# Optimization experiments

Hardware: AMD Instinct MI355X
Metric: run time of the kernel (lower is better)

Reference implementation:

```python
import jax, jax.numpy as jnp
import numpy as np

B, S, D, H = 2, 2048, 1024, 16
DK = D // H  # 64


def setup_inputs() -> dict:
    key = jax.random.key(0)
    ks = jax.random.split(key, 8)
    sc = 1.0 / np.sqrt(D)
    return {
        "q": jax.random.normal(ks[0], (B, S, D), jnp.float32),
        "k": jax.random.normal(ks[1], (B, S, D), jnp.float32),
        "v": jax.random.normal(ks[2], (B, S, D), jnp.float32),
        "Wq": jax.random.normal(ks[3], (D, D), jnp.float32) * sc,
        "bq": jnp.zeros((D,), jnp.float32),
        "Wk": jax.random.normal(ks[4], (D, D), jnp.float32) * sc,
        "bk": jnp.zeros((D,), jnp.float32),
        "Wv": jax.random.normal(ks[5], (D, D), jnp.float32) * sc,
        "bv": jnp.zeros((D,), jnp.float32),
        "Wo": jax.random.normal(ks[6], (D, D), jnp.float32) * sc,
        "bo": jnp.zeros((D,), jnp.float32),
    }


def _heads(x, W, b):
    # torch nn.Linear: x @ W.T + b, then view(bs,-1,H,DK).transpose(1,2)
    bsz, seq, _ = x.shape
    y = x @ W.T + b
    return y.reshape(bsz, seq, H, DK).transpose(0, 2, 1, 3)  # [B,H,S,DK]


def reference(q, k, v, Wq, bq, Wk, bk, Wv, bv, Wo, bo):
    qh = _heads(q, Wq, bq)
    kh = _heads(k, Wk, bk)
    vh = _heads(v, Wv, bv)
    # scores: [B,H,S,S]; intended scale 1/sqrt(d_k) (source passes tensor k as d_k by mistake)
    scores = jnp.einsum("bhqd,bhkd->bhqk", qh, kh) / jnp.sqrt(jnp.float32(DK))
    attn = jax.nn.softmax(scores, axis=-1)  # dropout is identity in eval
    ctx = jnp.einsum("bhqk,bhkd->bhqd", attn, vh)  # [B,H,S,DK]
    concat = ctx.transpose(0, 2, 1, 3).reshape(-1, H * DK)  # [B*S, D] (source flattens batch+seq)
    return concat @ Wo.T + bo
```

## Files before the change

### kernel.cpp

```cpp
#include <hip/hip_runtime.h>

typedef __attribute__((ext_vector_type(4))) float f32x4;
typedef __attribute__((ext_vector_type(8))) short short8;
typedef __attribute__((ext_vector_type(4))) unsigned short u16x4;
typedef __attribute__((ext_vector_type(2))) unsigned u32x2;
typedef __attribute__((ext_vector_type(4))) unsigned u32x4;

#define DEV static __device__ __forceinline__

#define BSZ 2
#define SEQ 2048
#define DMODEL 1024
#define NH 16
#define DKH 64
#define MROWS (BSZ*SEQ)
#define HEAD_ELEMS (BSZ*NH*SEQ*DKH)
#define WMAT_ELEMS (DMODEL*DMODEL)
#define QSCALE 0.18033688011111374f

DEV unsigned short f2bf(float f) {
    unsigned u = __builtin_bit_cast(unsigned, f);
    u += 0x7FFFu + ((u >> 16) & 1u);
    return (unsigned short)(u >> 16);
}

DEV unsigned cvtpk(float a, float b) {
    unsigned r;
    asm("v_cvt_pk_bf16_f32 %0, %1, %2" : "=v"(r) : "v"(a), "v"(b));
    return r;
}

DEV float fexp2(float x) {
#if __has_builtin(__builtin_amdgcn_exp2f)
    return __builtin_amdgcn_exp2f(x);
#else
    float r;
    asm("v_exp_f32 %0, %1\n\ts_nop 0" : "=v"(r) : "v"(x));
    return r;
#endif
}

DEV void gload16(const void* g, void* l) {
    __builtin_amdgcn_global_load_lds(
        (const __attribute__((address_space(1))) void*)g,
        (__attribute__((address_space(3))) void*)l, 16, 0, 0);
}

DEV void cfence() { asm volatile("" ::: "memory"); }

__global__ __launch_bounds__(256) void convall_kernel(
    const float* __restrict__ q, const float* __restrict__ k,
    const float* __restrict__ v,
    const float* __restrict__ Wq, const float* __restrict__ Wk,
    const float* __restrict__ Wv, const float* __restrict__ Wo,
    unsigned short* __restrict__ abf, unsigned short* __restrict__ wbf)
{
    const int z = blockIdx.y;
    const int i = (blockIdx.x * 256 + threadIdx.x) * 8;
    const float* src;
    unsigned short* dst;
    if (z < 3) {
        src = ((z == 0) ? q : (z == 1) ? k : v) + i;
        dst = abf + (size_t)z * HEAD_ELEMS + i;
    } else {
        const int mi = i >> 20;
        const int off = i & (WMAT_ELEMS - 1);
        src = ((mi == 0) ? Wq : (mi == 1) ? Wk : (mi == 2) ? Wv : Wo) + off;
        dst = wbf + i;
    }
    f32x4 a = *(const f32x4*)(src);
    f32x4 b = *(const f32x4*)(src + 4);
    u32x4 o;
    o[0] = cvtpk(a[0], a[1]); o[1] = cvtpk(a[2], a[3]);
    o[2] = cvtpk(b[0], b[1]); o[3] = cvtpk(b[2], b[3]);
    *(u32x4*)(dst) = o;
}

__global__ __launch_bounds__(256) void wconv_kernel(
    const float* __restrict__ Wq, const float* __restrict__ Wk,
    const float* __restrict__ Wv, const float* __restrict__ Wo,
    unsigned short* __restrict__ dst)
{
    const int z = blockIdx.y;
    const float* src = (z == 0) ? Wq : (z == 1) ? Wk : (z == 2) ? Wv : Wo;
    const int i = (blockIdx.x * 256 + threadIdx.x) * 4;
    f32x4 v = *(const f32x4*)(src + i);
    u16x4 o;
    o[0] = f2bf(v[0]); o[1] = f2bf(v[1]); o[2] = f2bf(v[2]); o[3] = f2bf(v[3]);
    *(u16x4*)(dst + (size_t)z * WMAT_ELEMS + i) = o;
}

__global__ __launch_bounds__(256) void aconv_kernel(
    const float* __restrict__ src, unsigned short* __restrict__ dst)
{
    const int i = (blockIdx.x * 256 + threadIdx.x) * 8;
    f32x4 a = *(const f32x4*)(src + i);
    f32x4 b = *(const f32x4*)(src + i + 4);
    u32x4 o;
    o[0] = cvtpk(a[0], a[1]); o[1] = cvtpk(a[2], a[3]);
    o[2] = cvtpk(b[0], b[1]); o[3] = cvtpk(b[2], b[3]);
    *(u32x4*)(dst + i) = o;
}

__global__ __launch_bounds__(256, 3) void proj_gemm_kernel(
    const unsigned short* __restrict__ Aq, const unsigned short* __restrict__ Ak,
    const unsigned short* __restrict__ Av,
    const unsigned short* __restrict__ Wbf,
    const float* __restrict__ bq, const float* __restrict__ bk, const float* __restrict__ bvv,
    unsigned short* __restrict__ heads, int zbase)
{
    const int z = zbase + blockIdx.z;
    const unsigned short* A = (z == 0) ? Aq : (z == 1) ? Ak : Av;
    const float* bias = (z == 0) ? bq : (z == 1) ? bk : bvv;
    const unsigned short* W = Wbf + (size_t)z * WMAT_ELEMS;
    unsigned short* outp = heads + (size_t)z * HEAD_ELEMS;

    __shared__ __align__(16) unsigned short As[128 * 64];
    __shared__ __align__(16) unsigned short Bs[128 * 64];

    const int tid = threadIdx.x;
    const int lane = tid & 63;
    const int w = tid >> 6;
    const int wr = w >> 1, wc = w & 1;
    const int l15 = lane & 15, l4 = lane >> 4;
    const int m0 = blockIdx.x * 128, n0 = blockIdx.y * 128;

    f32x4 acc[4][4];
    #pragma unroll
    for (int i = 0; i < 4; i++)
        #pragma unroll
        for (int j = 0; j < 4; j++) acc[i][j] = (f32x4){0.f, 0.f, 0.f, 0.f};

    const int srow = w * 8 + (lane >> 3);
    const int ssrc = ((lane & 7) ^ (srow & 7)) * 8;
    const unsigned short* ga = A + (size_t)(m0 + srow) * DMODEL + ssrc;
    const unsigned short* gb = W + (size_t)(n0 + srow) * DMODEL + ssrc;

    for (int k0 = 0; k0 < DMODEL; k0 += 64) {
        __syncthreads();
        #pragma unroll
        for (int c = 0; c < 4; c++) {
            gload16(ga + (size_t)c * 32 * DMODEL + k0, As + (c * 4 + w) * 512);
            gload16(gb + (size_t)c * 32 * DMODEL + k0, Bs + (c * 4 + w) * 512);
        }
        __syncthreads();

        short8 af[2][4], bf[2][4];
        #pragma unroll
        for (int mi = 0; mi < 4; mi++) {
            const int r = wr * 64 + mi * 16 + l15;
            const int x = r & 7;
            const char* base = (const char*)As + r * 128;
            af[0][mi] = *(const short8*)(base + ((l4 ^ x) << 4));
            af[1][mi] = *(const short8*)(base + (((4 + l4) ^ x) << 4));
        }
        #pragma unroll
        for (int ni = 0; ni < 4; ni++) {
            const int r = wc * 64 + ni * 16 + l15;
            const int x = r & 7;
            const char* base = (const char*)Bs + r * 128;
            bf[0][ni] = *(const short8*)(base + ((l4 ^ x) << 4));
            bf[1][ni] = *(const short8*)(base + (((4 + l4) ^ x) << 4));
        }

        __builtin_amdgcn_s_setprio(1);
        #pragma unroll
        for (int ks = 0; ks < 2; ks++)
            #pragma unroll
            for (int mi = 0; mi < 4; mi++)
                #pragma unroll
                for (int ni = 0; ni < 4; ni++)
                    acc[mi][ni] = __builtin_amdgcn_mfma_f32_16x16x32_bf16(
                        af[ks][mi], bf[ks][ni], acc[mi][ni], 0, 0, 0);
        __builtin_amdgcn_s_setprio(0);
    }

    if (z < 2) {
        const float sc = (z == 0) ? QSCALE : 1.0f;
        #pragma unroll
        for (int ni = 0; ni < 4; ni++) {
            const int n = n0 + wc * 64 + ni * 16 + l15;
            const float bn = bias[n];
            const int h = n >> 6, dk = n & 63;
            #pragma unroll
            for (int mi = 0; mi < 4; mi++) {
                #pragma unroll
                for (int r = 0; r < 4; r++) {
                    const int m = m0 + wr * 64 + mi * 16 + l4 * 4 + r;
                    const int b = m >> 11, s = m & 2047;
                    outp[((size_t)((b * NH + h) * SEQ) + s) * DKH + dk] =
                        f2bf((acc[mi][ni][r] + bn) * sc);
                }
            }
        }
    } else {
        #pragma unroll
        for (int ni = 0; ni < 4; ni++) {
            const int n = n0 + wc * 64 + ni * 16 + l15;
            const float bn = bias[n];
            const int h = n >> 6, dk = n & 63;
            #pragma unroll
            for (int mi = 0; mi < 4; mi++) {
                const int m = m0 + wr * 64 + mi * 16 + l4 * 4;
                const int b = m >> 11, s = m & 2047;
                float v0 = acc[mi][ni][0] + bn, v1 = acc[mi][ni][1] + bn;
                float v2 = acc[mi][ni][2] + bn, v3 = acc[mi][ni][3] + bn;
                u32x2 pk; pk[0] = cvtpk(v0, v1); pk[1] = cvtpk(v2, v3);
                *(u32x2*)(outp + ((size_t)((b * NH + h) * DKH + dk)) * SEQ + s) = pk;
            }
        }
    }
}

#define KVB 64
#define NTILES (SEQ/KVB)

__global__ __launch_bounds__(512, 2) void attn_kernel(
    const unsigned short* __restrict__ Qh, const unsigned short* __restrict__ Kh,
    const unsigned short* __restrict__ Vtg, unsigned short* __restrict__ Ctx)
{
    __shared__ __align__(16) char lds[65536];

    const int tid = threadIdx.x;
    const int lane = tid & 63, w = tid >> 6;
    const int l15 = lane & 15, l4 = lane >> 4;

    const int bid = blockIdx.x;
    const int bh = (bid & 7) * 4 + (bid >> 6);
    const int qt = (bid >> 3) & 7;
    const int q0 = qt * 256;

    const unsigned short* Qp = Qh + (size_t)bh * (SEQ * DKH);
    const unsigned short* Kp = Kh + (size_t)bh * (SEQ * DKH);
    const unsigned short* Vp = Vtg + (size_t)bh * (SEQ * DKH);
    char* Pw = lds + 32768 + w * 4096;

    const unsigned short* qrow = Qp + (size_t)(q0 + w * 32 + l15) * DKH + l4 * 8;
    const short8 qf0h0 = *(const short8*)(qrow);
    const short8 qf1h0 = *(const short8*)(qrow + 32);
    const short8 qf0h1 = *(const short8*)(qrow + 16 * DKH);
    const short8 qf1h1 = *(const short8*)(qrow + 16 * DKH + 32);

    const int srow = tid >> 3;
    const int sseg = ((tid & 7) ^ (srow & 7)) * 8;
    const unsigned short* kg = Kp + (size_t)srow * DKH + sseg;
    const unsigned short* vg = Vp + (size_t)srow * SEQ + sseg;

    float lsum0 = 0.f, lsum1 = 0.f;
    f32x4 o0[4], o1[4];
    #pragma unroll
    for (int d = 0; d < 4; d++) {
        o0[d] = (f32x4){0.f, 0.f, 0.f, 0.f};
        o1[d] = (f32x4){0.f, 0.f, 0.f, 0.f};
    }

    const int fb = l15 * 128 + ((l4 * 16) ^ ((l15 & 7) << 4));
    const int pswz = (l15 & 7) << 4;

    gload16(kg,         lds + w * 1024);
    gload16(vg, lds + 16384 + w * 1024);

    for (int t = 0; t < NTILES; ++t) {
        __syncthreads();
        const int cur = t & 1;

        if (t + 1 < NTILES) {
            gload16(kg + (size_t)(t + 1) * (KVB * DKH),
                    lds + (cur ^ 1) * 8192 + w * 1024);
            gload16(vg + (t + 1) * KVB,
                    lds + 16384 + (cur ^ 1) * 8192 + w * 1024);
        }

        const char* Kb = lds + cur * 8192;
        const char* Vb = lds + 16384 + cur * 8192;

        f32x4 s0[4], s1[4];
        #pragma unroll
        for (int nf = 0; nf < 4; nf++) {
            s0[nf] = (f32x4){0.f, 0.f, 0.f, 0.f};
            s1[nf] = (f32x4){0.f, 0.f, 0.f, 0.f};
        }
        __builtin_amdgcn_s_setprio(1);
        #pragma unroll
        for (int ks = 0; ks < 2; ks++) {
            const int fo = fb ^ (ks << 6);
            #pragma unroll
            for (int nf = 0; nf < 4; nf++) {
                short8 kf = *(const short8*)(Kb + fo + nf * 2048);
                s0[nf] = __builtin_amdgcn_mfma_f32_16x16x32_bf16(
                    kf, ks ? qf1h0 : qf0h0, s0[nf], 0, 0, 0);
                s1[nf] = __builtin_amdgcn_mfma_f32_16x16x32_bf16(
                    kf, ks ? qf1h1 : qf0h1, s1[nf], 0, 0, 0);
            }
        }
        __builtin_amdgcn_s_setprio(0);

        cfence();

        float ps0 = 0.f, ps1 = 0.f;
        #pragma unroll
        for (int nf = 0; nf < 4; nf++) {
            const float a0 = fexp2(s0[nf][0]), a1 = fexp2(s0[nf][1]);
            const float a2 = fexp2(s0[nf][2]), a3 = fexp2(s0[nf][3]);
            ps0 += (a0 + a1) + (a2 + a3);
            u32x2 pk0; pk0[0] = cvtpk(a0, a1); pk0[1] = cvtpk(a2, a3);
            *(u32x2*)(Pw + l15 * 128 + ((nf * 32 + l4 * 8) ^ pswz)) = pk0;

            const float b0 = fexp2(s1[nf][0]), b1 = fexp2(s1[nf][1]);
            const float b2 = fexp2(s1[nf][2]), b3 = fexp2(s1[nf][3]);
            ps1 += (b0 + b1) + (b2 + b3);
            u32x2 pk1; pk1[0] = cvtpk(b0, b1); pk1[1] = cvtpk(b2, b3);
            *(u32x2*)(Pw + 2048 + l15 * 128 + ((nf * 32 + l4 * 8) ^ pswz)) = pk1;
        }
        ps0 += __shfl_xor(ps0, 16); ps0 += __shfl_xor(ps0, 32); lsum0 += ps0;
        ps1 += __shfl_xor(ps1, 16); ps1 += __shfl_xor(ps1, 32); lsum1 += ps1;

        cfence();

        __builtin_amdgcn_s_setprio(1);
        #pragma unroll
        for (int ks = 0; ks < 2; ks++) {
            const int po = (ks * 64 + l4 * 16) ^ pswz;
            short8 pa0 = *(const short8*)(Pw + l15 * 128 + po);
            short8 pa1 = *(const short8*)(Pw + 2048 + l15 * 128 + po);
            const int fo = fb ^ (ks << 6);
            #pragma unroll
            for (int d = 0; d < 4; d++) {
                short8 vb = *(const short8*)(Vb + fo + d * 2048);
                o0[d] = __builtin_amdgcn_mfma_f32_16x16x32_bf16(pa0, vb, o0[d], 0, 0, 0);
                o1[d] = __builtin_amdgcn_mfma_f32_16x16x32_bf16(pa1, vb, o1[d], 0, 0, 0);
            }
        }
        __builtin_amdgcn_s_setprio(0);

        cfence();
    }

    const int b = bh >> 4, h = bh & 15;
    {
        const float linv = 1.f / lsum0;
        #pragma unroll
        for (int r = 0; r < 4; r++) {
            const float lr = __shfl(linv, l4 * 4 + r);
            const int sq = q0 + w * 32 + l4 * 4 + r;
            const size_t base = ((size_t)(b * SEQ + sq)) * DMODEL + h * DKH;
            #pragma unroll
            for (int d = 0; d < 4; d++)
                Ctx[base + d * 16 + l15] = f2bf(o0[d][r] * lr);
        }
    }
    {
        const float linv = 1.f / lsum1;
        #pragma unroll
        for (int r = 0; r < 4; r++) {
            const float lr = __shfl(linv, l4 * 4 + r);
            const int sq = q0 + w * 32 + 16 + l4 * 4 + r;
            const size_t base = ((size_t)(b * SEQ + sq)) * DMODEL + h * DKH;
            #pragma unroll
            for (int d = 0; d < 4; d++)
                Ctx[base + d * 16 + l15] = f2bf(o1[d][r] * lr);
        }
    }
}

__global__ __launch_bounds__(256, 3) void out_gemm_kernel(
    const unsigned short* __restrict__ Ctx, const unsigned short* __restrict__ Wobf,
    const float* __restrict__ bo, float* __restrict__ outp)
{
    __shared__ __align__(16) unsigned short As[128 * 64];
    __shared__ __align__(16) unsigned short Bs[128 * 64];

    const int tid = threadIdx.x;
    const int lane = tid & 63;
    const int w = tid >> 6;
    const int wr = w >> 1, wc = w & 1;
    const int l15 = lane & 15, l4 = lane >> 4;
    const int m0 = blockIdx.x * 128, n0 = blockIdx.y * 128;

    f32x4 acc[4][4];
    #pragma unroll
    for (int i = 0; i < 4; i++)
        #pragma unroll
        for (int j = 0; j < 4; j++) acc[i][j] = (f32x4){0.f, 0.f, 0.f, 0.f};

    const int srow = w * 8 + (lane >> 3);
    const int ssrc = ((lane & 7) ^ (srow & 7)) * 8;
    const unsigned short* ga = Ctx + (size_t)(m0 + srow) * DMODEL + ssrc;
    const unsigned short* gb = Wobf + (size_t)(n0 + srow) * DMODEL + ssrc;

    for (int k0 = 0; k0 < DMODEL; k0 += 64) {
        __syncthreads();
        #pragma unroll
        for (int c = 0; c < 4; c++) {
            gload16(ga + (size_t)c * 32 * DMODEL + k0, As + (c * 4 + w) * 512);
            gload16(gb + (size_t)c * 32 * DMODEL + k0, Bs + (c * 4 + w) * 512);
        }
        __syncthreads();

        short8 af[2][4], bf[2][4];
        #pragma unroll
        for (int mi = 0; mi < 4; mi++) {
            const int r = wr * 64 + mi * 16 + l15;
            const int x = r & 7;
            const char* base = (const char*)As + r * 128;
            af[0][mi] = *(const short8*)(base + ((l4 ^ x) << 4));
            af[1][mi] = *(const short8*)(base + (((4 + l4) ^ x) << 4));
        }
        #pragma unroll
        for (int ni = 0; ni < 4; ni++) {
            const int r = wc * 64 + ni * 16 + l15;
            const int x = r & 7;
            const char* base = (const char*)Bs + r * 128;
            bf[0][ni] = *(const short8*)(base + ((l4 ^ x) << 4));
            bf[1][ni] = *(const short8*)(base + (((4 + l4) ^ x) << 4));
        }

        __builtin_amdgcn_s_setprio(1);
        #pragma unroll
        for (int ks = 0; ks < 2; ks++)
            #pragma unroll
            for (int mi = 0; mi < 4; mi++)
                #pragma unroll
                for (int ni = 0; ni < 4; ni++)
                    acc[mi][ni] = __builtin_amdgcn_mfma_f32_16x16x32_bf16(
                        af[ks][mi], bf[ks][ni], acc[mi][ni], 0, 0, 0);
        __builtin_amdgcn_s_setprio(0);
    }

    #pragma unroll
    for (int ni = 0; ni < 4; ni++) {
        const int n = n0 + wc * 64 + ni * 16 + l15;
        const float bn = bo[n];
        #pragma unroll
        for (int mi = 0; mi < 4; mi++) {
            #pragma unroll
            for (int r = 0; r < 4; r++) {
                const int m = m0 + wr * 64 + mi * 16 + l4 * 4 + r;
                outp[(size_t)m * DMODEL + n] = acc[mi][ni][r] + bn;
            }
        }
    }
}

extern "C" void kernel_launch(void* const* d_in, const int* in_sizes, int n_in,
                              void* d_out, int out_size, void* d_ws, size_t ws_size,
                              hipStream_t stream)
{
    (void)in_sizes; (void)n_in; (void)out_size;
    const float* q  = (const float*)d_in[0];
    const float* k  = (const float*)d_in[1];
    const float* v  = (const float*)d_in[2];
    const float* Wq = (const float*)d_in[3];
    const float* bq = (const float*)d_in[4];
    const float* Wk = (const float*)d_in[5];
    const float* bk = (const float*)d_in[6];
    const float* Wv = (const float*)d_in[7];
    const float* bv = (const float*)d_in[8];
    const float* Wo = (const float*)d_in[9];
    const float* bo = (const float*)d_in[10];
    float* outp = (float*)d_out;

    unsigned short* ws  = (unsigned short*)d_ws;
    unsigned short* Wbf = ws;

    const size_t BIG_NEED = (size_t)(4u * WMAT_ELEMS + 6u * HEAD_ELEMS) * 2u;

    if (ws_size >= BIG_NEED) {
        unsigned short* qbf = ws + 4u * WMAT_ELEMS;
        unsigned short* kbf = qbf + HEAD_ELEMS;
        unsigned short* vbf = kbf + HEAD_ELEMS;
        unsigned short* Qh  = vbf + HEAD_ELEMS;
        unsigned short* Kh  = Qh + HEAD_ELEMS;
        unsigned short* Vt  = Kh + HEAD_ELEMS;
        unsigned short* Ctx = qbf;

        hipLaunchKernelGGL(convall_kernel, dim3(2048, 4), dim3(256), 0, stream,
                           q, k, v, Wq, Wk, Wv, Wo, qbf, Wbf);
        hipLaunchKernelGGL(proj_gemm_kernel, dim3(32, 8, 3), dim3(256), 0, stream,
                           qbf, kbf, vbf, Wbf, bq, bk, bv, Qh, 0);
        hipLaunchKernelGGL(attn_kernel, dim3(256), dim3(512), 0, stream,
                           Qh, Kh, Vt, Ctx);
        hipLaunchKernelGGL(out_gemm_kernel, dim3(32, 8), dim3(256), 0, stream,
                           Ctx, Wbf + 3u * WMAT_ELEMS, bo, outp);
    } else {
        unsigned short* Abf = ws + 4u * WMAT_ELEMS;
        unsigned short* Qh  = Abf + HEAD_ELEMS;
        unsigned short* Kh  = Qh + HEAD_ELEMS;
        unsigned short* Vt  = Kh + HEAD_ELEMS;
        unsigned short* Ctx = Abf;

        hipLaunchKernelGGL(wconv_kernel, dim3(1024, 4), dim3(256), 0, stream,
                           Wq, Wk, Wv, Wo, Wbf);
        const float* srcs[3] = {q, k, v};
        for (int z = 0; z < 3; z++) {
            hipLaunchKernelGGL(aconv_kernel, dim3(2048), dim3(256), 0, stream, srcs[z], Abf);
            hipLaunchKernelGGL(proj_gemm_kernel, dim3(32, 8, 1), dim3(256), 0, stream,
                               Abf, Abf, Abf, Wbf, bq, bk, bv, Qh, z);
        }
        hipLaunchKernelGGL(attn_kernel, dim3(256), dim3(512), 0, stream,
                           Qh, Kh, Vt, Ctx);
        hipLaunchKernelGGL(out_gemm_kernel, dim3(32, 8), dim3(256), 0, stream,
                           Ctx, Wbf + 3u * WMAT_ELEMS, bo, outp);
    }
}
```

Measured before the change: 106.3 us.

## Fuse fp32-to-bf16 activation conversion into projection GEMM A-tile loads

Removes the separate activation conversion kernel. The projection GEMM now reads fp32 q/k/v straight from global memory, packs them to bf16 in registers, and writes them swizzled into LDS, prefetching the next k-tile into registers during compute. This drops a full write and reread of the bf16 activation copies, but the A tile is now loaded through registers instead of async global-to-LDS loads, and each GEMM block rereads fp32 data (twice the bytes) across the 8 n-tiles. The workspace-size branch is also removed and a single layout is used.

```diff
diff --git a/kernel.cpp b/kernel.cpp
--- a/kernel.cpp
+++ b/kernel.cpp
@@ -47,34 +47,6 @@
 }
 
 DEV void cfence() { asm volatile("" ::: "memory"); }
-
-__global__ __launch_bounds__(256) void convall_kernel(
-    const float* __restrict__ q, const float* __restrict__ k,
-    const float* __restrict__ v,
-    const float* __restrict__ Wq, const float* __restrict__ Wk,
-    const float* __restrict__ Wv, const float* __restrict__ Wo,
-    unsigned short* __restrict__ abf, unsigned short* __restrict__ wbf)
-{
-    const int z = blockIdx.y;
-    const int i = (blockIdx.x * 256 + threadIdx.x) * 8;
-    const float* src;
-    unsigned short* dst;
-    if (z < 3) {
-        src = ((z == 0) ? q : (z == 1) ? k : v) + i;
-        dst = abf + (size_t)z * HEAD_ELEMS + i;
-    } else {
-        const int mi = i >> 20;
-        const int off = i & (WMAT_ELEMS - 1);
-        src = ((mi == 0) ? Wq : (mi == 1) ? Wk : (mi == 2) ? Wv : Wo) + off;
-        dst = wbf + i;
-    }
-    f32x4 a = *(const f32x4*)(src);
-    f32x4 b = *(const f32x4*)(src + 4);
-    u32x4 o;
-    o[0] = cvtpk(a[0], a[1]); o[1] = cvtpk(a[2], a[3]);
-    o[2] = cvtpk(b[0], b[1]); o[3] = cvtpk(b[2], b[3]);
-    *(u32x4*)(dst) = o;
-}
 
 __global__ __launch_bounds__(256) void wconv_kernel(
     const float* __restrict__ Wq, const float* __restrict__ Wk,
@@ -90,27 +62,15 @@
     *(u16x4*)(dst + (size_t)z * WMAT_ELEMS + i) = o;
 }
 
-__global__ __launch_bounds__(256) void aconv_kernel(
-    const float* __restrict__ src, unsigned short* __restrict__ dst)
-{
-    const int i = (blockIdx.x * 256 + threadIdx.x) * 8;
-    f32x4 a = *(const f32x4*)(src + i);
-    f32x4 b = *(const f32x4*)(src + i + 4);
-    u32x4 o;
-    o[0] = cvtpk(a[0], a[1]); o[1] = cvtpk(a[2], a[3]);
-    o[2] = cvtpk(b[0], b[1]); o[3] = cvtpk(b[2], b[3]);
-    *(u32x4*)(dst + i) = o;
-}
-
 __global__ __launch_bounds__(256, 3) void proj_gemm_kernel(
-    const unsigned short* __restrict__ Aq, const unsigned short* __restrict__ Ak,
-    const unsigned short* __restrict__ Av,
+    const float* __restrict__ Aq, const float* __restrict__ Ak,
+    const float* __restrict__ Av,
     const unsigned short* __restrict__ Wbf,
     const float* __restrict__ bq, const float* __restrict__ bk, const float* __restrict__ bvv,
-    unsigned short* __restrict__ heads, int zbase)
+    unsigned short* __restrict__ heads)
 {
-    const int z = zbase + blockIdx.z;
-    const unsigned short* A = (z == 0) ? Aq : (z == 1) ? Ak : Av;
+    const int z = blockIdx.z;
+    const float* A = (z == 0) ? Aq : (z == 1) ? Ak : Av;
     const float* bias = (z == 0) ? bq : (z == 1) ? bk : bvv;
     const unsigned short* W = Wbf + (size_t)z * WMAT_ELEMS;
     unsigned short* outp = heads + (size_t)z * HEAD_ELEMS;
@@ -131,19 +91,44 @@
         #pragma unroll
         for (int j = 0; j < 4; j++) acc[i][j] = (f32x4){0.f, 0.f, 0.f, 0.f};
 
+    const int ar = tid >> 1;
+    const int sb = (tid & 1) * 4;
+    const float* ga = A + (size_t)(m0 + ar) * DMODEL + sb * 8;
+    const int ax = ar & 7;
+    char* awr = (char*)As + ar * 128;
+
     const int srow = w * 8 + (lane >> 3);
     const int ssrc = ((lane & 7) ^ (srow & 7)) * 8;
-    const unsigned short* ga = A + (size_t)(m0 + srow) * DMODEL + ssrc;
     const unsigned short* gb = W + (size_t)(n0 + srow) * DMODEL + ssrc;
+
+    u32x4 aw[4];
+    #pragma unroll
+    for (int c = 0; c < 4; c++) {
+        f32x4 lo = *(const f32x4*)(ga + c * 8);
+        f32x4 hi = *(const f32x4*)(ga + c * 8 + 4);
+        aw[c][0] = cvtpk(lo[0], lo[1]); aw[c][1] = cvtpk(lo[2], lo[3]);
+        aw[c][2] = cvtpk(hi[0], hi[1]); aw[c][3] = cvtpk(hi[2], hi[3]);
+    }
 
     for (int k0 = 0; k0 < DMODEL; k0 += 64) {
         __syncthreads();
         #pragma unroll
-        for (int c = 0; c < 4; c++) {
-            gload16(ga + (size_t)c * 32 * DMODEL + k0, As + (c * 4 + w) * 512);
+        for (int c = 0; c < 4; c++)
+            *(u32x4*)(awr + (((sb + c) ^ ax) << 4)) = aw[c];
+        #pragma unroll
+        for (int c = 0; c < 4; c++)
             gload16(gb + (size_t)c * 32 * DMODEL + k0, Bs + (c * 4 + w) * 512);
-        }
         __syncthreads();
+
+        if (k0 + 64 < DMODEL) {
+            #pragma unroll
+            for (int c = 0; c < 4; c++) {
+                f32x4 lo = *(const f32x4*)(ga + k0 + 64 + c * 8);
+                f32x4 hi = *(const f32x4*)(ga + k0 + 64 + c * 8 + 4);
+                aw[c][0] = cvtpk(lo[0], lo[1]); aw[c][1] = cvtpk(lo[2], lo[3]);
+                aw[c][2] = cvtpk(hi[0], hi[1]); aw[c][3] = cvtpk(hi[2], hi[3]);
+            }
+        }
 
         short8 af[2][4], bf[2][4];
         #pragma unroll
@@ -446,7 +431,7 @@
                               void* d_out, int out_size, void* d_ws, size_t ws_size,
                               hipStream_t stream)
 {
-    (void)in_sizes; (void)n_in; (void)out_size;
+    (void)in_sizes; (void)n_in; (void)out_size; (void)ws_size;
     const float* q  = (const float*)d_in[0];
     const float* k  = (const float*)d_in[1];
     const float* v  = (const float*)d_in[2];
@@ -462,44 +447,17 @@
 
     unsigned short* ws  = (unsigned short*)d_ws;
     unsigned short* Wbf = ws;
-
-    const size_t BIG_NEED = (size_t)(4u * WMAT_ELEMS + 6u * HEAD_ELEMS) * 2u;
-
-    if (ws_size >= BIG_NEED) {
-        unsigned short* qbf = ws + 4u * WMAT_ELEMS;
-        unsigned short* kbf = qbf + HEAD_ELEMS;
-        unsigned short* vbf = kbf + HEAD_ELEMS;
-        unsigned short* Qh  = vbf + HEAD_ELEMS;
-        unsigned short* Kh  = Qh + HEAD_ELEMS;
-        unsigned short* Vt  = Kh + HEAD_ELEMS;
-        unsigned short* Ctx = qbf;
-
-        hipLaunchKernelGGL(convall_kernel, dim3(2048, 4), dim3(256), 0, stream,
-                           q, k, v, Wq, Wk, Wv, Wo, qbf, Wbf);
-        hipLaunchKernelGGL(proj_gemm_kernel, dim3(32, 8, 3), dim3(256), 0, stream,
-                           qbf, kbf, vbf, Wbf, bq, bk, bv, Qh, 0);
-        hipLaunchKernelGGL(attn_kernel, dim3(256), dim3(512), 0, stream,
-                           Qh, Kh, Vt, Ctx);
-        hipLaunchKernelGGL(out_gemm_kernel, dim3(32, 8), dim3(256), 0, stream,
-                           Ctx, Wbf + 3u * WMAT_ELEMS, bo, outp);
-    } else {
-        unsigned short* Abf = ws + 4u * WMAT_ELEMS;
-        unsigned short* Qh  = Abf + HEAD_ELEMS;
-        unsigned short* Kh  = Qh + HEAD_ELEMS;
-        unsigned short* Vt  = Kh + HEAD_ELEMS;
-        unsigned short* Ctx = Abf;
-
-        hipLaunchKernelGGL(wconv_kernel, dim3(1024, 4), dim3(256), 0, stream,
-                           Wq, Wk, Wv, Wo, Wbf);
-        const float* srcs[3] = {q, k, v};
-        for (int z = 0; z < 3; z++) {
-            hipLaunchKernelGGL(aconv_kernel, dim3(2048), dim3(256), 0, stream, srcs[z], Abf);
-            hipLaunchKernelGGL(proj_gemm_kernel, dim3(32, 8, 1), dim3(256), 0, stream,
-                               Abf, Abf, Abf, Wbf, bq, bk, bv, Qh, z);
-        }
-        hipLaunchKernelGGL(attn_kernel, dim3(256), dim3(512), 0, stream,
-                           Qh, Kh, Vt, Ctx);
-        hipLaunchKernelGGL(out_gemm_kernel, dim3(32, 8), dim3(256), 0, stream,
-                           Ctx, Wbf + 3u * WMAT_ELEMS, bo, outp);
-    }
-}
+    unsigned short* Qh  = ws + 4u * WMAT_ELEMS;
+    unsigned short* Kh  = Qh + HEAD_ELEMS;
+    unsigned short* Vt  = Kh + HEAD_ELEMS;
+    unsigned short* Ctx = Vt + HEAD_ELEMS;
+
+    hipLaunchKernelGGL(wconv_kernel, dim3(1024, 4), dim3(256), 0, stream,
+                       Wq, Wk, Wv, Wo, Wbf);
+    hipLaunchKernelGGL(proj_gemm_kernel, dim3(32, 8, 3), dim3(256), 0, stream,
+                       q, k, v, Wbf, bq, bk, bv, Qh);
+    hipLaunchKernelGGL(attn_kernel, dim3(256), dim3(512), 0, stream,
+                       Qh, Kh, Vt, Ctx);
+    hipLaunchKernelGGL(out_gemm_kernel, dim3(32, 8), dim3(256), 0, stream,
+                       Ctx, Wbf + 3u * WMAT_ELEMS, bo, outp);
+}
```

After: 132.7 us. 24.8% more time.
